# Optimization experiments

Hardware: AMD Instinct MI355X
Metric: run time of the kernel (lower is better)

The kernel has to match this reference:

```python
import jax, jax.numpy as jnp
import numpy as np

TEMPERATURE = 0.02


def setup_inputs() -> dict:
    key = jax.random.key(0)
    k1, k2 = jax.random.split(key)
    B, D_PER, DIM = 4096, 2, 1024
    # scale embeddings so sim/temperature stays in a sane range (like normalized embeddings)
    scale = 1.0 / np.sqrt(DIM)
    query_embeds = jax.random.normal(k1, (B, DIM), dtype=jnp.float32) * scale
    doc_embeds = jax.random.normal(k2, (B * D_PER, DIM), dtype=jnp.float32) * scale
    return {
        "query_embeds": query_embeds,
        "doc_embeds": doc_embeds,
        "num_docs_per_sample": D_PER,
    }


def reference(query_embeds, doc_embeds, num_docs_per_sample):
    # Single-device path of the original: all_doc_embeds == doc_embeds,
    # local_rank == 0, pos_global_idx = i * num_docs_per_sample.
    B = query_embeds.shape[0]
    # [B, total_docs] similarity matrix (one batched GEMM instead of per-sample loop)
    logits = (query_embeds @ doc_embeds.T) / TEMPERATURE
    pos_idx = jnp.arange(B) * num_docs_per_sample  # constant docs-per-sample offsets
    pos_logit = jnp.take_along_axis(logits, pos_idx[:, None], axis=1)[:, 0]
    lse = jax.nn.logsumexp(logits, axis=1)
    loss = jnp.sum(lse - pos_logit) / B
    return loss
```

## Files before the change

### kernel.cpp

```cpp
#include <hip/hip_runtime.h>


#define TEMP_INV 50.0f
#define PRESCALE 16.0f
#define SCALE_BYTE 123

typedef int   i32x4 __attribute__((ext_vector_type(4)));
typedef int   i32x8 __attribute__((ext_vector_type(8)));
typedef float f32x4 __attribute__((ext_vector_type(4)));

__global__ void cvt_kernel(const float* __restrict__ Q, const float* __restrict__ Dm,
                           unsigned int* __restrict__ Q8, unsigned int* __restrict__ D8,
                           float* __restrict__ rowsum, int qSlots, int B, int K) {
    const int gid = blockIdx.x * blockDim.x + threadIdx.x;
    if (gid < B) rowsum[gid] = 0.0f;
    const float* src;
    unsigned int* dst;
    int s;
    if (gid < qSlots) { src = Q;  dst = Q8; s = gid; }
    else              { src = Dm; dst = D8; s = gid - qSlots; }
    const int l   = s & 63;
    const int c   = (s >> 6) & 15;
    const int k0b = (s >> 10) & 7;
    const int R   = s >> 13;
    const int row = R * 128 + (c >> 1) * 16 + (l & 15);
    const int k   = k0b * 128 + (c & 1) * 64 + (l >> 4) * 16;
    const float* p = src + (size_t)row * K + k;
    unsigned int w[4];
#pragma unroll
    for (int d = 0; d < 4; ++d) {
        float4 v = *(const float4*)(p + d * 4);
        int t = __builtin_amdgcn_cvt_pk_fp8_f32(v.x * PRESCALE, v.y * PRESCALE, 0, false);
        t = __builtin_amdgcn_cvt_pk_fp8_f32(v.z * PRESCALE, v.w * PRESCALE, t, true);
        w[d] = (unsigned int)t;
    }
    *(uint4*)(dst + (size_t)s * 4) = make_uint4(w[0], w[1], w[2], w[3]);
}

__global__ __launch_bounds__(256, 2) void gemm_expsum_kernel(
        const unsigned int* __restrict__ Q8, const unsigned int* __restrict__ D8,
        const int* __restrict__ dper,
        float* __restrict__ rowsum, float* __restrict__ pos, int K) {
    __shared__ unsigned int Qs[4096];
    __shared__ unsigned int Ds[4096];

    const int tid   = threadIdx.x;
    const int wave  = tid >> 6;
    const int lane  = tid & 63;
    const int lquad = lane >> 4;
    const int lm    = lane & 15;
    const int qbase = blockIdx.x * 128;
    const int dbase = blockIdx.y * 128;
    const int KB    = K >> 7;

    const int slotofs = ((lquad & 1) * 32 + lm) * 4;
    const int aofs = ((wave >> 1) * 8 + (lquad >> 1)) * 256 + slotofs;
    const int bofs = ((wave & 1) * 8 + (lquad >> 1)) * 256 + slotofs;

    const unsigned int* Qg = Q8 + (size_t)blockIdx.x * KB * 4096;
    const unsigned int* Dg = D8 + (size_t)blockIdx.y * KB * 4096;

    f32x4 acc[16];
#pragma unroll
    for (int t = 0; t < 16; ++t) acc[t] = (f32x4){0.f, 0.f, 0.f, 0.f};

    for (int kb = 0; kb < KB; ++kb) {
#pragma unroll
        for (int q = 0; q < 4; ++q) {
            const int c = wave * 4 + q;
            const unsigned int* g1 = Qg + kb * 4096 + c * 256 + lane * 4;
            __builtin_amdgcn_global_load_lds(
                (const __attribute__((address_space(1))) void*)g1,
                (__attribute__((address_space(3))) void*)(Qs + c * 256 + lane * 4),
                16, 0, 0);
            const unsigned int* g2 = Dg + kb * 4096 + c * 256 + lane * 4;
            __builtin_amdgcn_global_load_lds(
                (const __attribute__((address_space(1))) void*)g2,
                (__attribute__((address_space(3))) void*)(Ds + c * 256 + lane * 4),
                16, 0, 0);
        }
        __syncthreads();

        i32x8 a8[4], b8[4];
#pragma unroll
        for (int i = 0; i < 4; ++i) {
            i32x4 lo = *(const i32x4*)(Qs + aofs + i * 512);
            i32x4 hi = *(const i32x4*)(Qs + aofs + i * 512 + 64);
            a8[i] = __builtin_shufflevector(lo, hi, 0, 1, 2, 3, 4, 5, 6, 7);
        }
#pragma unroll
        for (int j = 0; j < 4; ++j) {
            i32x4 lo = *(const i32x4*)(Ds + bofs + j * 512);
            i32x4 hi = *(const i32x4*)(Ds + bofs + j * 512 + 64);
            b8[j] = __builtin_shufflevector(lo, hi, 0, 1, 2, 3, 4, 5, 6, 7);
        }
#pragma unroll
        for (int i = 0; i < 4; ++i)
#pragma unroll
            for (int j = 0; j < 4; ++j)
                acc[i * 4 + j] = __builtin_amdgcn_mfma_scale_f32_16x16x128_f8f6f4(
                    a8[i], b8[j], acc[i * 4 + j], 0, 0, 0, SCALE_BYTE, 0, SCALE_BYTE);
        __syncthreads();
    }

    const int dp = dper[0];
#pragma unroll
    for (int i = 0; i < 4; ++i)
#pragma unroll
        for (int r = 0; r < 4; ++r) {
            const int gr   = qbase + (wave >> 1) * 64 + 16 * i + 4 * lquad + r;
            const int pcol = gr * dp - dbase;
            float e = 0.0f;
#pragma unroll
            for (int j = 0; j < 4; ++j) {
                float v = acc[i * 4 + j][r];
                if ((wave & 1) * 64 + 16 * j + lm == pcol) pos[gr] = v * TEMP_INV;
                e += __expf(v * TEMP_INV);
            }
            e += __shfl_xor(e, 1);
            e += __shfl_xor(e, 2);
            e += __shfl_xor(e, 4);
            e += __shfl_xor(e, 8);
            if (lm == 0) atomicAdd(&rowsum[gr], e);
        }
}

__global__ void final_kernel(const float* __restrict__ rowsum,
                             const float* __restrict__ pos,
                             float* __restrict__ out, int B) {
    __shared__ float red[16];
    int tid = threadIdx.x;
    float s = 0.0f;
    for (int i = tid; i < B; i += blockDim.x)
        s += __logf(rowsum[i]) - pos[i];
    s += __shfl_xor(s, 32);
    s += __shfl_xor(s, 16);
    s += __shfl_xor(s, 8);
    s += __shfl_xor(s, 4);
    s += __shfl_xor(s, 2);
    s += __shfl_xor(s, 1);
    int w = tid >> 6, l = tid & 63;
    if (l == 0) red[w] = s;
    __syncthreads();
    if (tid == 0) {
        float t = 0.0f;
        int nw = blockDim.x >> 6;
        for (int i = 0; i < nw; ++i) t += red[i];
        out[0] = t / (float)B;
    }
}

extern "C" void kernel_launch(void* const* d_in, const int* in_sizes, int n_in,
                              void* d_out, int out_size, void* d_ws, size_t ws_size,
                              hipStream_t stream) {
    const float* Q   = (const float*)d_in[0];
    const float* Dm  = (const float*)d_in[1];
    const int* dper  = (const int*)d_in[2];
    float* out = (float*)d_out;

    const int DIM  = 1024;
    const int B    = in_sizes[0] / DIM;
    const int Ntot = in_sizes[1] / DIM;

    unsigned int* Q8 = (unsigned int*)d_ws;
    unsigned int* D8 = Q8 + (size_t)B * DIM / 4;
    float* rowsum = (float*)(D8 + (size_t)Ntot * DIM / 4);
    float* pos = rowsum + B;

    const int qSlots = B * DIM / 16;
    const int dSlots = Ntot * DIM / 16;
    cvt_kernel<<<(qSlots + dSlots) / 256, 256, 0, stream>>>(
        Q, Dm, Q8, D8, rowsum, qSlots, B, DIM);

    dim3 grid(B / 128, Ntot / 128);
    gemm_expsum_kernel<<<grid, 256, 0, stream>>>(Q8, D8, dper, rowsum, pos, DIM);

    final_kernel<<<1, 1024, 0, stream>>>(rowsum, pos, out, B);
}
```

Baseline: 131.1 us.

## Use 256x256 tiles with 32x32x64 FP8 MFMA and double-buffered LDS

Rewrites the GEMM main loop to compute a 256x256 output tile per 512-thread block, using 32x32x64 scaled FP8 MFMAs instead of 16x16x128. Global-to-LDS loads are double-buffered over 64-wide K steps with explicit vmcnt waits, so the next tile loads while the current one is multiplied. MFMA sections also raise wave priority. The larger tile cuts global and LDS traffic per FLOP, but the grid shrinks to a quarter of the blocks and register pressure rises with 8 accumulators of 16 floats each.

```diff
diff --git a/kernel.cpp b/kernel.cpp
--- a/kernel.cpp
+++ b/kernel.cpp
@@ -7,7 +7,7 @@
 
 typedef int   i32x4 __attribute__((ext_vector_type(4)));
 typedef int   i32x8 __attribute__((ext_vector_type(8)));
-typedef float f32x4 __attribute__((ext_vector_type(4)));
+typedef float f32x16 __attribute__((ext_vector_type(16)));
 
 __global__ void cvt_kernel(const float* __restrict__ Q, const float* __restrict__ Dm,
                            unsigned int* __restrict__ Q8, unsigned int* __restrict__ D8,
@@ -37,91 +37,121 @@
     *(uint4*)(dst + (size_t)s * 4) = make_uint4(w[0], w[1], w[2], w[3]);
 }
 
-__global__ __launch_bounds__(256, 2) void gemm_expsum_kernel(
+__global__ __launch_bounds__(512, 2) void gemm_expsum_kernel(
         const unsigned int* __restrict__ Q8, const unsigned int* __restrict__ D8,
         const int* __restrict__ dper,
         float* __restrict__ rowsum, float* __restrict__ pos, int K) {
-    __shared__ unsigned int Qs[4096];
-    __shared__ unsigned int Ds[4096];
-
-    const int tid   = threadIdx.x;
-    const int wave  = tid >> 6;
-    const int lane  = tid & 63;
-    const int lquad = lane >> 4;
-    const int lm    = lane & 15;
-    const int qbase = blockIdx.x * 128;
-    const int dbase = blockIdx.y * 128;
-    const int KB    = K >> 7;
-
-    const int slotofs = ((lquad & 1) * 32 + lm) * 4;
-    const int aofs = ((wave >> 1) * 8 + (lquad >> 1)) * 256 + slotofs;
-    const int bofs = ((wave & 1) * 8 + (lquad >> 1)) * 256 + slotofs;
-
-    const unsigned int* Qg = Q8 + (size_t)blockIdx.x * KB * 4096;
-    const unsigned int* Dg = D8 + (size_t)blockIdx.y * KB * 4096;
-
-    f32x4 acc[16];
-#pragma unroll
-    for (int t = 0; t < 16; ++t) acc[t] = (f32x4){0.f, 0.f, 0.f, 0.f};
-
-    for (int kb = 0; kb < KB; ++kb) {
-#pragma unroll
-        for (int q = 0; q < 4; ++q) {
-            const int c = wave * 4 + q;
-            const unsigned int* g1 = Qg + kb * 4096 + c * 256 + lane * 4;
-            __builtin_amdgcn_global_load_lds(
-                (const __attribute__((address_space(1))) void*)g1,
-                (__attribute__((address_space(3))) void*)(Qs + c * 256 + lane * 4),
-                16, 0, 0);
-            const unsigned int* g2 = Dg + kb * 4096 + c * 256 + lane * 4;
-            __builtin_amdgcn_global_load_lds(
-                (const __attribute__((address_space(1))) void*)g2,
-                (__attribute__((address_space(3))) void*)(Ds + c * 256 + lane * 4),
-                16, 0, 0);
-        }
-        __syncthreads();
-
-        i32x8 a8[4], b8[4];
+    __shared__ unsigned int BUF[16384];
+
+    const int tid  = threadIdx.x;
+    const int wave = tid >> 6;
+    const int lane = tid & 63;
+    const int wr   = wave >> 2;
+    const int wc   = wave & 3;
+    const int lm   = lane & 15;
+    const int lh   = (lane >> 4) & 1;
+    const int hh   = lane >> 5;
+    const int l32  = lane & 31;
+    const int bx   = blockIdx.x, by = blockIdx.y;
+    const int KB8  = K >> 7;
+    const int KT   = K >> 6;
+
+    const unsigned int* srcq[4];
+    int dofs[4];
+#pragma unroll
+    for (int q = 0; q < 4; ++q) {
+        const int flat = wave * 4 + q;
+        const unsigned int* img;
+        if (flat < 16)
+            img = Q8 + (size_t)(2 * bx + (flat >> 3)) * KB8 * 4096;
+        else
+            img = D8 + (size_t)(2 * by + ((flat >> 3) & 1)) * KB8 * 4096;
+        srcq[q] = img + (flat & 7) * 512 + lane * 4;
+        dofs[q] = flat * 256 + lane * 4;
+    }
+
+#define STAGE(t) do { \
+    unsigned int* db_ = BUF + ((t) & 1) * 8192; \
+    const int so_ = ((t) >> 1) * 4096 + ((t) & 1) * 256; \
+    _Pragma("unroll") \
+    for (int q = 0; q < 4; ++q) \
+        __builtin_amdgcn_global_load_lds( \
+            (const __attribute__((address_space(1))) void*)(srcq[q] + so_), \
+            (__attribute__((address_space(3))) void*)(db_ + dofs[q]), 16, 0, 0); \
+    } while (0)
+
+    const int sl4 = (hh * 32 + lm) * 4;
+    int aoffs[4], boffs[2];
+#pragma unroll
+    for (int i = 0; i < 4; ++i)
+        aoffs[i] = (wr * 8 + i * 2 + lh) * 256 + sl4;
+#pragma unroll
+    for (int j = 0; j < 2; ++j)
+        boffs[j] = 4096 + ((wc >> 1) * 8 + (wc & 1) * 4 + j * 2 + lh) * 256 + sl4;
+
+    f32x16 acc[8];
+#pragma unroll
+    for (int t = 0; t < 8; ++t)
+#pragma unroll
+        for (int e = 0; e < 16; ++e) acc[t][e] = 0.0f;
+
+    STAGE(0);
+    for (int t = 0; t < KT; ++t) {
+        if (t + 1 < KT) {
+            STAGE(t + 1);
+            asm volatile("s_waitcnt vmcnt(4)" ::: "memory");
+        } else {
+            asm volatile("s_waitcnt vmcnt(0)" ::: "memory");
+        }
+        __builtin_amdgcn_s_barrier();
+
+        const unsigned int* bp = BUF + (t & 1) * 8192;
+        i32x8 a8[4], b8[2];
+#pragma unroll
+        for (int j = 0; j < 2; ++j) {
+            i32x4 lo = *(const i32x4*)(bp + boffs[j]);
+            i32x4 hi = *(const i32x4*)(bp + boffs[j] + 64);
+            b8[j] = __builtin_shufflevector(lo, hi, 0, 1, 2, 3, 4, 5, 6, 7);
+        }
 #pragma unroll
         for (int i = 0; i < 4; ++i) {
-            i32x4 lo = *(const i32x4*)(Qs + aofs + i * 512);
-            i32x4 hi = *(const i32x4*)(Qs + aofs + i * 512 + 64);
+            i32x4 lo = *(const i32x4*)(bp + aoffs[i]);
+            i32x4 hi = *(const i32x4*)(bp + aoffs[i] + 64);
             a8[i] = __builtin_shufflevector(lo, hi, 0, 1, 2, 3, 4, 5, 6, 7);
         }
-#pragma unroll
-        for (int j = 0; j < 4; ++j) {
-            i32x4 lo = *(const i32x4*)(Ds + bofs + j * 512);
-            i32x4 hi = *(const i32x4*)(Ds + bofs + j * 512 + 64);
-            b8[j] = __builtin_shufflevector(lo, hi, 0, 1, 2, 3, 4, 5, 6, 7);
-        }
+        __builtin_amdgcn_s_setprio(1);
 #pragma unroll
         for (int i = 0; i < 4; ++i)
 #pragma unroll
-            for (int j = 0; j < 4; ++j)
-                acc[i * 4 + j] = __builtin_amdgcn_mfma_scale_f32_16x16x128_f8f6f4(
-                    a8[i], b8[j], acc[i * 4 + j], 0, 0, 0, SCALE_BYTE, 0, SCALE_BYTE);
-        __syncthreads();
-    }
-
-    const int dp = dper[0];
+            for (int j = 0; j < 2; ++j)
+                acc[i * 2 + j] = __builtin_amdgcn_mfma_scale_f32_32x32x64_f8f6f4(
+                    a8[i], b8[j], acc[i * 2 + j], 0, 0, 0, SCALE_BYTE, 0, SCALE_BYTE);
+        __builtin_amdgcn_s_setprio(0);
+        __builtin_amdgcn_s_barrier();
+    }
+#undef STAGE
+
+    const int dp  = dper[0];
+    const int gr0 = bx * 256 + wr * 128 + 4 * hh;
+    const int gc0 = by * 256 + wc * 64 + l32;
 #pragma unroll
     for (int i = 0; i < 4; ++i)
 #pragma unroll
-        for (int r = 0; r < 4; ++r) {
-            const int gr   = qbase + (wave >> 1) * 64 + 16 * i + 4 * lquad + r;
-            const int pcol = gr * dp - dbase;
+        for (int r = 0; r < 16; ++r) {
+            const int gr = gr0 + i * 32 + (r & 3) + 8 * (r >> 2);
             float e = 0.0f;
 #pragma unroll
-            for (int j = 0; j < 4; ++j) {
-                float v = acc[i * 4 + j][r];
-                if ((wave & 1) * 64 + 16 * j + lm == pcol) pos[gr] = v * TEMP_INV;
-                e += __expf(v * TEMP_INV);
+            for (int j = 0; j < 2; ++j) {
+                float v = acc[i * 2 + j][r] * TEMP_INV;
+                if (gr * dp == gc0 + j * 32) pos[gr] = v;
+                e += __expf(v);
             }
             e += __shfl_xor(e, 1);
             e += __shfl_xor(e, 2);
             e += __shfl_xor(e, 4);
             e += __shfl_xor(e, 8);
-            if (lm == 0) atomicAdd(&rowsum[gr], e);
+            e += __shfl_xor(e, 16);
+            if (l32 == 0) atomicAdd(&rowsum[gr], e);
         }
 }
 
@@ -172,8 +202,8 @@
     cvt_kernel<<<(qSlots + dSlots) / 256, 256, 0, stream>>>(
         Q, Dm, Q8, D8, rowsum, qSlots, B, DIM);
 
-    dim3 grid(B / 128, Ntot / 128);
-    gemm_expsum_kernel<<<grid, 256, 0, stream>>>(Q8, D8, dper, rowsum, pos, DIM);
+    dim3 grid(B / 256, Ntot / 256);
+    gemm_expsum_kernel<<<grid, 512, 0, stream>>>(Q8, D8, dper, rowsum, pos, DIM);
 
     final_kernel<<<1, 1024, 0, stream>>>(rowsum, pos, out, B);
 }
```

New measurement: 182.2 us. 39.0% more time.

## Double-buffer LDS tiles in FP8 GEMM and coalesce conversion reads

Applied to the files above, without the earlier changes.

The GEMM main loop now uses two LDS buffers per operand. The global-to-LDS loads for the next K block are issued after the current fragments are read into registers, so the loads overlap with the MFMA work and one barrier per iteration is removed. The conversion kernel permutes the lane-to-slot mapping so that neighbouring threads read contiguous floats of the same row, which should coalesce its global reads but scatters its writes within each 1 KB chunk. Doubling LDS use per block may limit occupancy.

```diff
diff --git a/kernel.cpp b/kernel.cpp
--- a/kernel.cpp
+++ b/kernel.cpp
@@ -19,6 +19,10 @@
     int s;
     if (gid < qSlots) { src = Q;  dst = Q8; s = gid; }
     else              { src = Dm; dst = D8; s = gid - qSlots; }
+    {
+        const int l0 = s & 63;
+        s = (s & ~63) | (((l0 & 3) << 4) | (l0 >> 2));
+    }
     const int l   = s & 63;
     const int c   = (s >> 6) & 15;
     const int k0b = (s >> 10) & 7;
@@ -41,8 +45,10 @@
         const unsigned int* __restrict__ Q8, const unsigned int* __restrict__ D8,
         const int* __restrict__ dper,
         float* __restrict__ rowsum, float* __restrict__ pos, int K) {
-    __shared__ unsigned int Qs[4096];
-    __shared__ unsigned int Ds[4096];
+    __shared__ unsigned int Qs0[4096];
+    __shared__ unsigned int Ds0[4096];
+    __shared__ unsigned int Qs1[4096];
+    __shared__ unsigned int Ds1[4096];
 
     const int tid   = threadIdx.x;
     const int wave  = tid >> 6;
@@ -64,44 +70,51 @@
 #pragma unroll
     for (int t = 0; t < 16; ++t) acc[t] = (f32x4){0.f, 0.f, 0.f, 0.f};
 
-    for (int kb = 0; kb < KB; ++kb) {
-#pragma unroll
-        for (int q = 0; q < 4; ++q) {
-            const int c = wave * 4 + q;
-            const unsigned int* g1 = Qg + kb * 4096 + c * 256 + lane * 4;
-            __builtin_amdgcn_global_load_lds(
-                (const __attribute__((address_space(1))) void*)g1,
-                (__attribute__((address_space(3))) void*)(Qs + c * 256 + lane * 4),
-                16, 0, 0);
-            const unsigned int* g2 = Dg + kb * 4096 + c * 256 + lane * 4;
-            __builtin_amdgcn_global_load_lds(
-                (const __attribute__((address_space(1))) void*)g2,
-                (__attribute__((address_space(3))) void*)(Ds + c * 256 + lane * 4),
-                16, 0, 0);
-        }
-        __syncthreads();
+#define STAGE(kb_, QD, DD) do {                                              \
+    _Pragma("unroll")                                                        \
+    for (int q = 0; q < 4; ++q) {                                            \
+        const int c_ = wave * 4 + q;                                         \
+        __builtin_amdgcn_global_load_lds(                                    \
+            (const __attribute__((address_space(1))) void*)(Qg + (kb_) * 4096 + c_ * 256 + lane * 4), \
+            (__attribute__((address_space(3))) void*)(QD + c_ * 256 + lane * 4), 16, 0, 0); \
+        __builtin_amdgcn_global_load_lds(                                    \
+            (const __attribute__((address_space(1))) void*)(Dg + (kb_) * 4096 + c_ * 256 + lane * 4), \
+            (__attribute__((address_space(3))) void*)(DD + c_ * 256 + lane * 4), 16, 0, 0); \
+    }                                                                        \
+} while (0)
 
-        i32x8 a8[4], b8[4];
-#pragma unroll
-        for (int i = 0; i < 4; ++i) {
-            i32x4 lo = *(const i32x4*)(Qs + aofs + i * 512);
-            i32x4 hi = *(const i32x4*)(Qs + aofs + i * 512 + 64);
-            a8[i] = __builtin_shufflevector(lo, hi, 0, 1, 2, 3, 4, 5, 6, 7);
-        }
-#pragma unroll
-        for (int j = 0; j < 4; ++j) {
-            i32x4 lo = *(const i32x4*)(Ds + bofs + j * 512);
-            i32x4 hi = *(const i32x4*)(Ds + bofs + j * 512 + 64);
-            b8[j] = __builtin_shufflevector(lo, hi, 0, 1, 2, 3, 4, 5, 6, 7);
-        }
-#pragma unroll
-        for (int i = 0; i < 4; ++i)
-#pragma unroll
-            for (int j = 0; j < 4; ++j)
-                acc[i * 4 + j] = __builtin_amdgcn_mfma_scale_f32_16x16x128_f8f6f4(
-                    a8[i], b8[j], acc[i * 4 + j], 0, 0, 0, SCALE_BYTE, 0, SCALE_BYTE);
-        __syncthreads();
+#define KSTEP(kb_, QS, DS, QN, DN, doStage) do {                             \
+    i32x8 a8[4], b8[4];                                                      \
+    _Pragma("unroll")                                                        \
+    for (int i = 0; i < 4; ++i) {                                            \
+        i32x4 lo = *(const i32x4*)(QS + aofs + i * 512);                     \
+        i32x4 hi = *(const i32x4*)(QS + aofs + i * 512 + 64);                \
+        a8[i] = __builtin_shufflevector(lo, hi, 0, 1, 2, 3, 4, 5, 6, 7);     \
+    }                                                                        \
+    _Pragma("unroll")                                                        \
+    for (int j = 0; j < 4; ++j) {                                            \
+        i32x4 lo = *(const i32x4*)(DS + bofs + j * 512);                     \
+        i32x4 hi = *(const i32x4*)(DS + bofs + j * 512 + 64);                \
+        b8[j] = __builtin_shufflevector(lo, hi, 0, 1, 2, 3, 4, 5, 6, 7);     \
+    }                                                                        \
+    if (doStage) STAGE((kb_) + 1, QN, DN);                                   \
+    _Pragma("unroll")                                                        \
+    for (int i = 0; i < 4; ++i)                                              \
+        _Pragma("unroll")                                                    \
+        for (int j = 0; j < 4; ++j)                                          \
+            acc[i * 4 + j] = __builtin_amdgcn_mfma_scale_f32_16x16x128_f8f6f4( \
+                a8[i], b8[j], acc[i * 4 + j], 0, 0, 0, SCALE_BYTE, 0, SCALE_BYTE); \
+    __syncthreads();                                                         \
+} while (0)
+
+    STAGE(0, Qs0, Ds0);
+    __syncthreads();
+    for (int kb = 0; kb < KB; kb += 2) {
+        KSTEP(kb,     Qs0, Ds0, Qs1, Ds1, true);
+        KSTEP(kb + 1, Qs1, Ds1, Qs0, Ds0, kb + 2 < KB);
     }
+#undef KSTEP
+#undef STAGE
 
     const int dp = dper[0];
 #pragma unroll
```

Measured after the change: 136.8 us. +4.4%, slower.
